# Optimization experiments

Measured on AMD Instinct MI355X. Metric: run time of the kernel, lower is better.

The kernel has to match this reference:

```python
import jax, jax.numpy as jnp
import numpy as np
from jax import lax

GAMMA = 1.0
INF = 1000000.0  # matches the TF code's pseudo-infinity


def _pairwise_sq_dists(a, b):
    # ||a_i - b_j||^2 = ||a||^2 + ||b||^2 - 2 a.b ; avoids the [B,N,M,d] diff tensor
    a2 = jnp.sum(a * a, axis=-1)                      # (B, N)
    b2 = jnp.sum(b * b, axis=-1)                      # (B, M)
    ab = jnp.einsum('bnd,bmd->bnm', a, b)             # (B, N, M)
    return a2[:, :, None] + b2[:, None, :] - 2.0 * ab


def _soft_dtw(seq_a, seq_b, gamma):
    D = _pairwise_sq_dists(seq_a, seq_b)              # (B, N, M)
    B, N, M = D.shape
    dtype = D.dtype
    # row 0 of the DP table: R[0,0]=0, R[0,j>0]=INF
    row0 = jnp.full((B, M + 1), INF, dtype=dtype).at[:, 0].set(0.0)

    def row_step(prev_row, d_i):
        # prev_row: (B, M+1) = R[i-1, :]; d_i: (B, M) = D[:, i-1, :]
        def col_step(left, inputs):
            diag, up, d = inputs                      # each (B,)
            r = jnp.stack([diag, up, left], axis=-1)  # (B, 3)
            softmin = -gamma * jax.nn.logsumexp(-r / gamma, axis=-1)
            val = d + softmin
            return val, val
        left0 = jnp.full((B,), INF, dtype=dtype)      # R[i, 0] = INF
        xs = (prev_row[:, :-1].T, prev_row[:, 1:].T, d_i.T)  # scan over M
        _, vals = lax.scan(col_step, left0, xs)       # (M, B)
        new_row = jnp.concatenate([jnp.full((B, 1), INF, dtype=dtype), vals.T], axis=1)
        return new_row, None

    final_row, _ = lax.scan(row_step, row0, jnp.moveaxis(D, 1, 0))
    return final_row[:, -1]                           # R[N, M]


def setup_inputs() -> dict:
    key = jax.random.key(0)
    k1, k2 = jax.random.split(key)
    B, N, M, d = 128, 384, 384, 128
    seq_a = jax.random.normal(k1, (B, N, d), dtype=jnp.float32)
    seq_b = jax.random.normal(k2, (B, M, d), dtype=jnp.float32)
    return {"seq_a": seq_a, "seq_b": seq_b}


def reference(seq_a, seq_b):
    dist = _soft_dtw(seq_a, seq_b, GAMMA)
    return dist[:, None]                              # (B, 1)
```

## Files before the change

kernel.cpp:

```cpp
#include <hip/hip_runtime.h>
#include <stdint.h>

#define BATCH 128
#define SEQN  384
#define SEQM  384
#define DIM   128
#define KINF   1000000.0f
#define LOG2E  1.4426950408889634f
#define LN2    0.6931471805599453f
#define KINF2  (KINF * LOG2E)
#define NCOLS  388

#define OFF1   162
#define SLACK  17
#define RBMASK 63

#define EXP2F(x) __builtin_amdgcn_exp2f(x)
#define LOG2F(x) __builtin_amdgcn_logf(x)

#define WG __HIP_MEMORY_SCOPE_WORKGROUP

typedef __attribute__((ext_vector_type(8))) short bf16x8;
typedef __attribute__((ext_vector_type(4))) float f32x4;

__device__ __forceinline__ unsigned short bf16_rne(float x) {
    uint32_t u = __float_as_uint(x);
    u += 0x7FFFu + ((u >> 16) & 1u);
    return (unsigned short)(u >> 16);
}
__device__ __forceinline__ uint32_t bf16_pair(float x, float y) {
    uint32_t ux = __float_as_uint(x); ux += 0x7FFFu + ((ux >> 16) & 1u);
    uint32_t uy = __float_as_uint(y); uy += 0x7FFFu + ((uy >> 16) & 1u);
    return (ux >> 16) | (uy & 0xFFFF0000u);
}

union frag_u { bf16x8 v; uint32_t u[4]; };
struct us3 { unsigned short u[3]; };

#define SPIN_NZ(addr)                                                        \
    { int g_ = 0;                                                            \
      while (__hip_atomic_load((addr), __ATOMIC_ACQUIRE, WG) == 0)           \
          if (++g_ > (1 << 20)) break; }
#define SPIN_GE(addr, val)                                                   \
    { int g_ = 0;                                                            \
      while (__hip_atomic_load((addr), __ATOMIC_ACQUIRE, WG) < (val))        \
          if (++g_ > (1 << 20)) break; }

__global__ __launch_bounds__(320) void fused_dtw(
        const float* __restrict__ A, const float* __restrict__ B,
        unsigned short* __restrict__ Dt, float* __restrict__ out) {
    __shared__ __align__(16) unsigned short ldsA[SEQN][DIM];
    __shared__ __align__(16) float normA[SEQN];
    __shared__ __align__(8)  float bring[128];
    __shared__ int prod_done[16];
    __shared__ int w0_prog, w1_prog, stage_cnt;

    const int bat  = blockIdx.x;
    const int tid  = threadIdx.x;
    const int wv   = tid >> 6;
    const int lane = tid & 63;

    if (tid < 16) prod_done[tid] = 0;
    if (tid == 16) w0_prog = -1;
    if (tid == 17) w1_prog = -1;
    if (tid == 18) stage_cnt = 0;
    __syncthreads();

    unsigned short* __restrict__ DtB = Dt + (long)bat * NCOLS * SEQN;

    if (wv >= 2) {
        const int pt = tid - 128;
        const float* __restrict__ Ab = A + (long)bat * SEQN * DIM;
        const float* __restrict__ Bb = B + (long)bat * SEQM * DIM;

        for (int sp = 0; sp < 8; sp++) {
            float4 v0[4], v1[4];
            #pragma unroll
            for (int j = 0; j < 4; j++) {
                int e = (sp * 4 + j) * 1536 + pt * 8;
                v0[j] = *(const float4*)(Ab + e);
                v1[j] = *(const float4*)(Ab + e + 4);
            }
            #pragma unroll
            for (int j = 0; j < 4; j++) {
                int e   = (sp * 4 + j) * 1536 + pt * 8;
                int row = e >> 7;
                int grp = (e >> 3) & 15;
                int sw  = (grp ^ (row & 15)) * 8;
                uint4 va;
                va.x = bf16_pair(v0[j].x, v0[j].y); va.y = bf16_pair(v0[j].z, v0[j].w);
                va.z = bf16_pair(v1[j].x, v1[j].y); va.w = bf16_pair(v1[j].z, v1[j].w);
                *(uint4*)&ldsA[row][sw] = va;
                float sa = v0[j].x*v0[j].x + v0[j].y*v0[j].y + v0[j].z*v0[j].z + v0[j].w*v0[j].w
                         + v1[j].x*v1[j].x + v1[j].y*v1[j].y + v1[j].z*v1[j].z + v1[j].w*v1[j].w;
                #pragma unroll
                for (int off = 8; off > 0; off >>= 1) sa += __shfl_down(sa, off, 16);
                if ((pt & 15) == 0) normA[row] = sa;
            }
        }
        if (lane == 0) __hip_atomic_fetch_add(&stage_cnt, 1, __ATOMIC_RELEASE, WG);
        SPIN_GE(&stage_cnt, 3);

        const int l16 = lane & 15, q = lane >> 4;
        for (int k = wv - 2; k < 13; k += 3) {
            if (k == 12) {
                uint32_t pv = bf16_pair(KINF2, KINF2);
                #pragma unroll
                for (int c = 0; c < 4; c++) {
                    uint32_t* p = (uint32_t*)(DtB + (long)(384 + c) * SEQN + 6 * lane);
                    p[0] = pv; p[1] = pv; p[2] = pv;
                }
            } else {
                frag_u bfrag[2][4];
                float bn[2];
                #pragma unroll
                for (int jg = 0; jg < 2; jg++) {
                    const float* bp = Bb + (long)(32 * k + jg * 16 + l16) * DIM + q * 8;
                    float s = 0.0f;
                    #pragma unroll
                    for (int kk = 0; kk < 4; kk++) {
                        float4 w0 = *(const float4*)(bp + kk * 32);
                        float4 w1 = *(const float4*)(bp + kk * 32 + 4);
                        bfrag[jg][kk].u[0] = bf16_pair(w0.x, w0.y);
                        bfrag[jg][kk].u[1] = bf16_pair(w0.z, w0.w);
                        bfrag[jg][kk].u[2] = bf16_pair(w1.x, w1.y);
                        bfrag[jg][kk].u[3] = bf16_pair(w1.z, w1.w);
                        s += w0.x*w0.x + w0.y*w0.y + w0.z*w0.z + w0.w*w0.w
                           + w1.x*w1.x + w1.y*w1.y + w1.z*w1.z + w1.w*w1.w;
                    }
                    s += __shfl_xor(s, 16, 64);
                    s += __shfl_xor(s, 32, 64);
                    bn[jg] = s;
                }
                for (int si = 0; si < 24; si++) {
                    const int arow = si * 16 + l16;
                    frag_u afr[4];
                    #pragma unroll
                    for (int kk = 0; kk < 4; kk++)
                        afr[kk].v = *(const bf16x8*)&ldsA[arow][((kk * 4 + q) ^ (arow & 15)) * 8];
                    f32x4 acc0 = {0.0f, 0.0f, 0.0f, 0.0f};
                    f32x4 acc1 = {0.0f, 0.0f, 0.0f, 0.0f};
                    #pragma unroll
                    for (int kk = 0; kk < 4; kk++) {
                        acc0 = __builtin_amdgcn_mfma_f32_16x16x32_bf16(
                                   afr[kk].v, bfrag[0][kk].v, acc0, 0, 0, 0);
                        acc1 = __builtin_amdgcn_mfma_f32_16x16x32_bf16(
                                   afr[kk].v, bfrag[1][kk].v, acc1, 0, 0, 0);
                    }
                    float4 an = *(const float4*)&normA[si * 16 + q * 4];
                    #pragma unroll
                    for (int jg = 0; jg < 2; jg++) {
                        int col = 32 * k + jg * 16 + l16;
                        f32x4 ac = jg ? acc1 : acc0;
                        ushort4 pk;
                        pk.x = bf16_rne((an.x + bn[jg] - 2.0f * ac[0]) * LOG2E);
                        pk.y = bf16_rne((an.y + bn[jg] - 2.0f * ac[1]) * LOG2E);
                        pk.z = bf16_rne((an.z + bn[jg] - 2.0f * ac[2]) * LOG2E);
                        pk.w = bf16_rne((an.w + bn[jg] - 2.0f * ac[3]) * LOG2E);
                        *(ushort4*)(DtB + (long)col * SEQN + si * 16 + q * 4) = pk;
                    }
                }
            }
            if (lane == 0)
                __hip_atomic_store(&prod_done[k], 1, __ATOMIC_RELEASE, WG);
        }
        return;
    }

    const int  cw    = wv;
    const int  t     = lane;
    const bool isl0  = (t == 0);
    const int  off   = cw ? OFF1 : 0;
    const int  npair = cw ? 168 : 160;
    const unsigned short* __restrict__ dtb = DtB + 192 * cw + 3 * t;

    SPIN_NZ(&prod_done[0]);

    float prev[3];
    #pragma unroll
    for (int r = 0; r < 3; r++) prev[r] = KINF2;

    us3 dslot[4];
    #pragma unroll
    for (int qq = 0; qq < 4; qq++) {
        int c = qq - 2 * t - off;
        int cc = c < 0 ? 0 : c;
        long base = (long)cc * SEQN;
        dslot[qq].u[0] = dtb[base];
        dslot[qq].u[1] = dtb[base + 1];
        dslot[qq].u[2] = dtb[base + 2];
    }

    float rcv0 = KINF2, rcv1 = KINF2, old_diag = KINF2;
    float lane0_diag = cw ? KINF2 : 0.0f;
    float b_rcv0 = KINF2, b_rcv1 = KINF2, b_old = KINF2;
    float botA = KINF2, botB = KINF2;
    int c0 = -2 * t - off;
    int kdone = 0;

#define UNPACK3(d, w)                                                       \
    d[0] = __uint_as_float(((uint32_t)w.u[0]) << 16);                       \
    d[1] = __uint_as_float(((uint32_t)w.u[1]) << 16);                       \
    d[2] = __uint_as_float(((uint32_t)w.u[2]) << 16);

#define COLPASS(dX, diag0, upseed, LEFTV, NEWV)                             \
    {                                                                       \
        float Bp = (upseed), Fp = 1.0f;                                     \
        float Bv[3], Fv[3];                                                 \
        _Pragma("unroll")                                                   \
        for (int r = 0; r < 3; r++) {                                       \
            float vd = (r == 0) ? (diag0) : LEFTV[r - 1];                   \
            float vl = LEFTV[r];                                            \
            float m3 = fminf(fminf(vd, vl), Bp);            \
            float al = EXP2F(m3 - Bp);                                      \
            float be = EXP2F(m3 - vd) + EXP2F(m3 - vl);                     \
            float Fr = __builtin_fmaf(al, Fp, be);                          \
            float Br = dX[r] + m3;                                          \
            Bv[r] = Br; Fv[r] = Fr;                                         \
            Bp = Br; Fp = Fr;                                               \
        }                                                                   \
        _Pragma("unroll")                                                   \
        for (int r = 0; r < 3; r++)                                         \
            NEWV[r] = Bv[r] - LOG2F(Fv[r]);                                 \
    }

#define PHASE2(Q)                                                           \
    {                                                                       \
        us3 wA = dslot[Q];                                                  \
        us3 wB = dslot[(Q) + 1];                                            \
        {                \
            int cnA = c0 + 4;                                               \
            int ccA = cnA < 0 ? 0 : (cnA > 387 ? 387 : cnA);                \
            int cnB = c0 + 5;                                               \
            int ccB = cnB < 0 ? 0 : (cnB > 387 ? 387 : cnB);                \
            long bA = (long)ccA * SEQN;                                     \
            long bB = (long)ccB * SEQN;                                     \
            dslot[Q].u[0]       = dtb[bA];                                  \
            dslot[Q].u[1]       = dtb[bA + 1];                              \
            dslot[Q].u[2]       = dtb[bA + 2];                              \
            dslot[(Q) + 1].u[0] = dtb[bB];                                  \
            dslot[(Q) + 1].u[1] = dtb[bB + 1];                              \
            dslot[(Q) + 1].u[2] = dtb[bB + 2];                              \
        }                                                                   \
        float dA[3], dB[3];                                                 \
        UNPACK3(dA, wA)                                                     \
        UNPACK3(dB, wB)                                                     \
        float dgA = isl0 ? (cw ? b_old  : lane0_diag) : old_diag;           \
        float upA = isl0 ? (cw ? b_rcv0 : KINF2)      : rcv0;               \
        float upB = isl0 ? (cw ? b_rcv1 : KINF2)      : rcv1;               \
        float newA[3];                                                      \
        COLPASS(dA, dgA, upA, prev, newA)                                   \
        COLPASS(dB, upA, upB, newA, prev)                                   \
        old_diag = rcv1;                                                    \
        rcv0 = __shfl_up(newA[2], 1, 64);                                   \
        rcv1 = __shfl_up(prev[2], 1, 64);                                   \
        botA = newA[2]; botB = prev[2];                                     \
        lane0_diag = KINF2;                                                 \
        c0 += 2;                                                            \
    }

#define TAIL0(m)                                                            \
    {                                                                       \
        if (t == 63) {                                                      \
            *(float2*)&bring[((m) & RBMASK) * 2] = make_float2(botA, botB); \
            if (((m) & 7) == 7)                                             \
                __hip_atomic_store(&w0_prog, (m), __ATOMIC_RELEASE, WG);    \
        }                                                                   \
    }
#define TAIL1(n)                                                            \
    {                                                                       \
        b_old = b_rcv1;                                                     \
        if ((n) >= SLACK) {                                                 \
            float2 bv = *(float2*)&bring[(((n) - SLACK) & RBMASK) * 2];     \
            b_rcv0 = bv.x; b_rcv1 = bv.y;                                   \
        } else { b_rcv0 = KINF2; b_rcv1 = KINF2; }                          \
        if (((n) & 7) == 7 && t == 63)                                      \
            __hip_atomic_store(&w1_prog, (n), __ATOMIC_RELEASE, WG);        \
    }

    for (int p = 0; p < npair; p++) {
        if ((p & 3) == 3) {
            int kr = (4 * p + 19 - off) >> 5;
            if (kr > 12) kr = 12;
            if (kr > kdone) { SPIN_NZ(&prod_done[kr]); kdone = kr; }
            if (cw) {
                int thr = 2 * p - 10;
                if (thr > 318) thr = 318;
                if (thr >= 0) SPIN_GE(&w0_prog, thr);
            } else {
                int thr = 2 * p - 40;
                if (thr >= 0) SPIN_GE(&w1_prog, thr);
            }
        }
        PHASE2(0)
        if (cw == 0) TAIL0(2 * p) else TAIL1(2 * p)
        PHASE2(2)
        if (cw == 0) TAIL0(2 * p + 1) else TAIL1(2 * p + 1)
    }
#undef PHASE2
#undef COLPASS
#undef UNPACK3
#undef TAIL0
#undef TAIL1

    if (cw == 1 && t == 63) out[bat] = prev[2] * LN2;
}

extern "C" void kernel_launch(void* const* d_in, const int* in_sizes, int n_in,
                              void* d_out, int out_size, void* d_ws, size_t ws_size,
                              hipStream_t stream) {
    (void)in_sizes; (void)n_in; (void)out_size; (void)ws_size;
    const float* a = (const float*)d_in[0];
    const float* b = (const float*)d_in[1];
    float* out = (float*)d_out;

    unsigned short* Dmat = (unsigned short*)d_ws;

    fused_dtw<<<dim3(BATCH), dim3(320), 0, stream>>>(a, b, Dmat, out);
}
```

Baseline: 218.9 us.

## Split each batch's DTW across two workgroups with global boundary exchange

```diff
diff --git a/kernel.cpp b/kernel.cpp
--- a/kernel.cpp
+++ b/kernel.cpp
@@ -9,16 +9,18 @@
 #define LOG2E  1.4426950408889634f
 #define LN2    0.6931471805599453f
 #define KINF2  (KINF * LOG2E)
-#define NCOLS  388
-
+
+#define HCOLS  388
+#define CSTR   200
 #define OFF1   162
 #define SLACK  17
-#define RBMASK 63
+#define BND_SLOTS 512
 
 #define EXP2F(x) __builtin_amdgcn_exp2f(x)
 #define LOG2F(x) __builtin_amdgcn_logf(x)
 
 #define WG __HIP_MEMORY_SCOPE_WORKGROUP
+#define AG __HIP_MEMORY_SCOPE_AGENT
 
 typedef __attribute__((ext_vector_type(8))) short bf16x8;
 typedef __attribute__((ext_vector_type(4))) float f32x4;
@@ -36,79 +38,43 @@
 
 union frag_u { bf16x8 v; uint32_t u[4]; };
 struct us3 { unsigned short u[3]; };
-
-#define SPIN_NZ(addr)                                                        \
-    { int g_ = 0;                                                            \
-      while (__hip_atomic_load((addr), __ATOMIC_ACQUIRE, WG) == 0)           \
-          if (++g_ > (1 << 20)) break; }
-#define SPIN_GE(addr, val)                                                   \
-    { int g_ = 0;                                                            \
-      while (__hip_atomic_load((addr), __ATOMIC_ACQUIRE, WG) < (val))        \
-          if (++g_ > (1 << 20)) break; }
-
-__global__ __launch_bounds__(320) void fused_dtw(
+union BU { float2 f; unsigned long long u; };
+
+__global__ __launch_bounds__(256) void fused_dtw(
         const float* __restrict__ A, const float* __restrict__ B,
-        unsigned short* __restrict__ Dt, float* __restrict__ out) {
-    __shared__ __align__(16) unsigned short ldsA[SEQN][DIM];
-    __shared__ __align__(16) float normA[SEQN];
-    __shared__ __align__(8)  float bring[128];
+        unsigned long long* __restrict__ bnd, int* __restrict__ w0prog,
+        float* __restrict__ out) {
+    __shared__ __align__(16) unsigned short ldsD[HCOLS * CSTR];
+    __shared__ __align__(16) float normA[192];
     __shared__ int prod_done[16];
-    __shared__ int w0_prog, w1_prog, stage_cnt;
-
-    const int bat  = blockIdx.x;
+
+    const int bx   = blockIdx.x;
+    const int bat  = bx >> 1;
+    const int h    = bx & 1;
     const int tid  = threadIdx.x;
     const int wv   = tid >> 6;
     const int lane = tid & 63;
 
     if (tid < 16) prod_done[tid] = 0;
-    if (tid == 16) w0_prog = -1;
-    if (tid == 17) w1_prog = -1;
-    if (tid == 18) stage_cnt = 0;
     __syncthreads();
 
-    unsigned short* __restrict__ DtB = Dt + (long)bat * NCOLS * SEQN;
-
-    if (wv >= 2) {
-        const int pt = tid - 128;
-        const float* __restrict__ Ab = A + (long)bat * SEQN * DIM;
+    unsigned long long* __restrict__ bndB = bnd + (long)bat * BND_SLOTS;
+    int* __restrict__ w0p = w0prog + bat;
+
+    if (wv != 0) {
+        const int l16 = lane & 15, q = lane >> 4;
+        const int sbase = (wv - 1) * 4;
+        const float* __restrict__ Ab = A + ((long)bat * SEQN + 192 * h) * DIM;
         const float* __restrict__ Bb = B + (long)bat * SEQM * DIM;
-
-        for (int sp = 0; sp < 8; sp++) {
-            float4 v0[4], v1[4];
-            #pragma unroll
-            for (int j = 0; j < 4; j++) {
-                int e = (sp * 4 + j) * 1536 + pt * 8;
-                v0[j] = *(const float4*)(Ab + e);
-                v1[j] = *(const float4*)(Ab + e + 4);
-            }
-            #pragma unroll
-            for (int j = 0; j < 4; j++) {
-                int e   = (sp * 4 + j) * 1536 + pt * 8;
-                int row = e >> 7;
-                int grp = (e >> 3) & 15;
-                int sw  = (grp ^ (row & 15)) * 8;
-                uint4 va;
-                va.x = bf16_pair(v0[j].x, v0[j].y); va.y = bf16_pair(v0[j].z, v0[j].w);
-                va.z = bf16_pair(v1[j].x, v1[j].y); va.w = bf16_pair(v1[j].z, v1[j].w);
-                *(uint4*)&ldsA[row][sw] = va;
-                float sa = v0[j].x*v0[j].x + v0[j].y*v0[j].y + v0[j].z*v0[j].z + v0[j].w*v0[j].w
-                         + v1[j].x*v1[j].x + v1[j].y*v1[j].y + v1[j].z*v1[j].z + v1[j].w*v1[j].w;
-                #pragma unroll
-                for (int off = 8; off > 0; off >>= 1) sa += __shfl_down(sa, off, 16);
-                if ((pt & 15) == 0) normA[row] = sa;
-            }
-        }
-        if (lane == 0) __hip_atomic_fetch_add(&stage_cnt, 1, __ATOMIC_RELEASE, WG);
-        SPIN_GE(&stage_cnt, 3);
-
-        const int l16 = lane & 15, q = lane >> 4;
-        for (int k = wv - 2; k < 13; k += 3) {
+        bool first = true;
+        for (int k = 0; k < 13; k++) {
             if (k == 12) {
-                uint32_t pv = bf16_pair(KINF2, KINF2);
-                #pragma unroll
-                for (int c = 0; c < 4; c++) {
-                    uint32_t* p = (uint32_t*)(DtB + (long)(384 + c) * SEQN + 6 * lane);
-                    p[0] = pv; p[1] = pv; p[2] = pv;
+                if (wv == 1) {
+                    uint32_t pv = bf16_pair(KINF2, KINF2);
+                    int c = lane >> 4, i16 = lane & 15;
+                    uint32_t* p = (uint32_t*)&ldsD[(384 + c) * CSTR] + i16 * 6;
+                    #pragma unroll
+                    for (int j = 0; j < 6; j++) p[j] = pv;
                 }
             } else {
                 frag_u bfrag[2][4];
@@ -132,12 +98,47 @@
                     s += __shfl_xor(s, 32, 64);
                     bn[jg] = s;
                 }
-                for (int si = 0; si < 24; si++) {
-                    const int arow = si * 16 + l16;
+                float4 c0v[4], c1v[4];
+                {
+                    const float* ap = Ab + (long)(sbase * 16 + l16) * DIM + q * 8;
+                    #pragma unroll
+                    for (int kk = 0; kk < 4; kk++) {
+                        c0v[kk] = *(const float4*)(ap + kk * 32);
+                        c1v[kk] = *(const float4*)(ap + kk * 32 + 4);
+                    }
+                }
+                #pragma unroll
+                for (int s4 = 0; s4 < 4; s4++) {
+                    const int si = sbase + s4;
+                    float4 n0[4], n1[4];
+                    if (s4 < 3) {
+                        const float* ap = Ab + (long)((si + 1) * 16 + l16) * DIM + q * 8;
+                        #pragma unroll
+                        for (int kk = 0; kk < 4; kk++) {
+                            n0[kk] = *(const float4*)(ap + kk * 32);
+                            n1[kk] = *(const float4*)(ap + kk * 32 + 4);
+                        }
+                    }
                     frag_u afr[4];
                     #pragma unroll
-                    for (int kk = 0; kk < 4; kk++)
-                        afr[kk].v = *(const bf16x8*)&ldsA[arow][((kk * 4 + q) ^ (arow & 15)) * 8];
+                    for (int kk = 0; kk < 4; kk++) {
+                        afr[kk].u[0] = bf16_pair(c0v[kk].x, c0v[kk].y);
+                        afr[kk].u[1] = bf16_pair(c0v[kk].z, c0v[kk].w);
+                        afr[kk].u[2] = bf16_pair(c1v[kk].x, c1v[kk].y);
+                        afr[kk].u[3] = bf16_pair(c1v[kk].z, c1v[kk].w);
+                    }
+                    if (first) {
+                        float sa = 0.0f;
+                        #pragma unroll
+                        for (int kk = 0; kk < 4; kk++)
+                            sa += c0v[kk].x*c0v[kk].x + c0v[kk].y*c0v[kk].y
+                                + c0v[kk].z*c0v[kk].z + c0v[kk].w*c0v[kk].w
+                                + c1v[kk].x*c1v[kk].x + c1v[kk].y*c1v[kk].y
+                                + c1v[kk].z*c1v[kk].z + c1v[kk].w*c1v[kk].w;
+                        sa += __shfl_xor(sa, 16, 64);
+                        sa += __shfl_xor(sa, 32, 64);
+                        if (q == 0) normA[si * 16 + l16] = sa;
+                    }
                     f32x4 acc0 = {0.0f, 0.0f, 0.0f, 0.0f};
                     f32x4 acc1 = {0.0f, 0.0f, 0.0f, 0.0f};
                     #pragma unroll
@@ -147,6 +148,7 @@
                         acc1 = __builtin_amdgcn_mfma_f32_16x16x32_bf16(
                                    afr[kk].v, bfrag[1][kk].v, acc1, 0, 0, 0);
                     }
+                    if (first) asm volatile("s_waitcnt lgkmcnt(0)" ::: "memory");
                     float4 an = *(const float4*)&normA[si * 16 + q * 4];
                     #pragma unroll
                     for (int jg = 0; jg < 2; jg++) {
@@ -157,24 +159,30 @@
                         pk.y = bf16_rne((an.y + bn[jg] - 2.0f * ac[1]) * LOG2E);
                         pk.z = bf16_rne((an.z + bn[jg] - 2.0f * ac[2]) * LOG2E);
                         pk.w = bf16_rne((an.w + bn[jg] - 2.0f * ac[3]) * LOG2E);
-                        *(ushort4*)(DtB + (long)col * SEQN + si * 16 + q * 4) = pk;
-                    }
-                }
+                        *(ushort4*)&ldsD[col * CSTR + si * 16 + q * 4] = pk;
+                    }
+                    if (s4 < 3) {
+                        #pragma unroll
+                        for (int kk = 0; kk < 4; kk++) { c0v[kk] = n0[kk]; c1v[kk] = n1[kk]; }
+                    }
+                }
+                first = false;
             }
             if (lane == 0)
-                __hip_atomic_store(&prod_done[k], 1, __ATOMIC_RELEASE, WG);
+                __hip_atomic_fetch_add(&prod_done[k], 1, __ATOMIC_RELEASE, WG);
         }
         return;
     }
 
-    const int  cw    = wv;
     const int  t     = lane;
     const bool isl0  = (t == 0);
-    const int  off   = cw ? OFF1 : 0;
-    const int  npair = cw ? 168 : 160;
-    const unsigned short* __restrict__ dtb = DtB + 192 * cw + 3 * t;
-
-    SPIN_NZ(&prod_done[0]);
+    const int  off   = h ? OFF1 : 0;
+    const int  npair = h ? 168 : 160;
+    const unsigned short* __restrict__ ldsT = ldsD + 3 * t;
+
+    {   int g = 0;
+        while (__hip_atomic_load(&prod_done[0], __ATOMIC_ACQUIRE, WG) < 3)
+            if (++g > (1 << 20)) break; }
 
     float prev[3];
     #pragma unroll
@@ -185,18 +193,18 @@
     for (int qq = 0; qq < 4; qq++) {
         int c = qq - 2 * t - off;
         int cc = c < 0 ? 0 : c;
-        long base = (long)cc * SEQN;
-        dslot[qq].u[0] = dtb[base];
-        dslot[qq].u[1] = dtb[base + 1];
-        dslot[qq].u[2] = dtb[base + 2];
+        const unsigned short* p = ldsT + cc * CSTR;
+        dslot[qq].u[0] = p[0]; dslot[qq].u[1] = p[1]; dslot[qq].u[2] = p[2];
     }
 
     float rcv0 = KINF2, rcv1 = KINF2, old_diag = KINF2;
-    float lane0_diag = cw ? KINF2 : 0.0f;
+    float lane0_diag = h ? KINF2 : 0.0f;
     float b_rcv0 = KINF2, b_rcv1 = KINF2, b_old = KINF2;
     float botA = KINF2, botB = KINF2;
+    float2 bq0, bq1, bq2, bq3;
+    bq0 = bq1 = bq2 = bq3 = make_float2(KINF2, KINF2);
     int c0 = -2 * t - off;
-    int kdone = 0;
+    int kdone = 0, w0seen = -1;
 
 #define UNPACK3(d, w)                                                       \
     d[0] = __uint_as_float(((uint32_t)w.u[0]) << 16);                       \
@@ -228,26 +236,26 @@
     {                                                                       \
         us3 wA = dslot[Q];                                                  \
         us3 wB = dslot[(Q) + 1];                                            \
-        {                \
+        {                     \
             int cnA = c0 + 4;                                               \
             int ccA = cnA < 0 ? 0 : (cnA > 387 ? 387 : cnA);                \
             int cnB = c0 + 5;                                               \
             int ccB = cnB < 0 ? 0 : (cnB > 387 ? 387 : cnB);                \
-            long bA = (long)ccA * SEQN;                                     \
-            long bB = (long)ccB * SEQN;                                     \
-            dslot[Q].u[0]       = dtb[bA];                                  \
-            dslot[Q].u[1]       = dtb[bA + 1];                              \
-            dslot[Q].u[2]       = dtb[bA + 2];                              \
-            dslot[(Q) + 1].u[0] = dtb[bB];                                  \
-            dslot[(Q) + 1].u[1] = dtb[bB + 1];                              \
-            dslot[(Q) + 1].u[2] = dtb[bB + 2];                              \
+            const unsigned short* pA = ldsT + ccA * CSTR;                   \
+            const unsigned short* pB = ldsT + ccB * CSTR;                   \
+            dslot[Q].u[0]       = pA[0];                                    \
+            dslot[Q].u[1]       = pA[1];                                    \
+            dslot[Q].u[2]       = pA[2];                                    \
+            dslot[(Q) + 1].u[0] = pB[0];                                    \
+            dslot[(Q) + 1].u[1] = pB[1];                                    \
+            dslot[(Q) + 1].u[2] = pB[2];                                    \
         }                                                                   \
         float dA[3], dB[3];                                                 \
         UNPACK3(dA, wA)                                                     \
         UNPACK3(dB, wB)                                                     \
-        float dgA = isl0 ? (cw ? b_old  : lane0_diag) : old_diag;           \
-        float upA = isl0 ? (cw ? b_rcv0 : KINF2)      : rcv0;               \
-        float upB = isl0 ? (cw ? b_rcv1 : KINF2)      : rcv1;               \
+        float dgA = isl0 ? (h ? b_old  : lane0_diag) : old_diag;            \
+        float upA = isl0 ? (h ? b_rcv0 : KINF2)      : rcv0;                \
+        float upB = isl0 ? (h ? b_rcv1 : KINF2)      : rcv1;                \
         float newA[3];                                                      \
         COLPASS(dA, dgA, upA, prev, newA)                                   \
         COLPASS(dB, upA, upB, newA, prev)                                   \
@@ -262,40 +270,52 @@
 #define TAIL0(m)                                                            \
     {                                                                       \
         if (t == 63) {                                                      \
-            *(float2*)&bring[((m) & RBMASK) * 2] = make_float2(botA, botB); \
+            BU bu; bu.f = make_float2(botA, botB);                          \
+            __hip_atomic_store(&bndB[m], bu.u, __ATOMIC_RELAXED, AG);       \
             if (((m) & 7) == 7)                                             \
-                __hip_atomic_store(&w0_prog, (m), __ATOMIC_RELEASE, WG);    \
+                __hip_atomic_store(w0p, (m), __ATOMIC_RELEASE, AG);         \
         }                                                                   \
     }
 #define TAIL1(n)                                                            \
     {                                                                       \
         b_old = b_rcv1;                                                     \
-        if ((n) >= SLACK) {                                                 \
-            float2 bv = *(float2*)&bring[(((n) - SLACK) & RBMASK) * 2];     \
-            b_rcv0 = bv.x; b_rcv1 = bv.y;                                   \
-        } else { b_rcv0 = KINF2; b_rcv1 = KINF2; }                          \
-        if (((n) & 7) == 7 && t == 63)                                      \
-            __hip_atomic_store(&w1_prog, (n), __ATOMIC_RELEASE, WG);        \
+        if ((n) >= SLACK) { b_rcv0 = bq0.x; b_rcv1 = bq0.y; }               \
+        else              { b_rcv0 = KINF2; b_rcv1 = KINF2; }               \
+        bq0 = bq1; bq1 = bq2; bq2 = bq3;                                    \
+        int sl = (n) + 4 - SLACK;                                           \
+        if (sl >= 0) {                                                      \
+            BU bu;                                                          \
+            bu.u = __hip_atomic_load(&bndB[sl], __ATOMIC_RELAXED, AG);      \
+            bq3 = bu.f;                                                     \
+        }                                                                   \
     }
 
     for (int p = 0; p < npair; p++) {
         if ((p & 3) == 3) {
             int kr = (4 * p + 19 - off) >> 5;
             if (kr > 12) kr = 12;
-            if (kr > kdone) { SPIN_NZ(&prod_done[kr]); kdone = kr; }
-            if (cw) {
-                int thr = 2 * p - 10;
-                if (thr > 318) thr = 318;
-                if (thr >= 0) SPIN_GE(&w0_prog, thr);
-            } else {
-                int thr = 2 * p - 40;
-                if (thr >= 0) SPIN_GE(&w1_prog, thr);
+            if (kr > kdone) {
+                int g = 0;
+                while (__hip_atomic_load(&prod_done[kr], __ATOMIC_ACQUIRE, WG) < 3)
+                    if (++g > (1 << 20)) break;
+                kdone = kr;
+            }
+            if (h) {
+                int thr = 2 * p - 6;
+                if (thr > 319) thr = 319;
+                if (thr >= 0 && w0seen < thr) {
+                    int g = 0, v = w0seen;
+                    do {
+                        v = __hip_atomic_load(w0p, __ATOMIC_ACQUIRE, AG);
+                    } while (v < thr && ++g < (1 << 20));
+                    w0seen = v;
+                }
             }
         }
         PHASE2(0)
-        if (cw == 0) TAIL0(2 * p) else TAIL1(2 * p)
+        if (h == 0) { TAIL0(2 * p) } else { TAIL1(2 * p) }
         PHASE2(2)
-        if (cw == 0) TAIL0(2 * p + 1) else TAIL1(2 * p + 1)
+        if (h == 0) { TAIL0(2 * p + 1) } else { TAIL1(2 * p + 1) }
     }
 #undef PHASE2
 #undef COLPASS
@@ -303,7 +323,7 @@
 #undef TAIL0
 #undef TAIL1
 
-    if (cw == 1 && t == 63) out[bat] = prev[2] * LN2;
+    if (h == 1 && t == 63) out[bat] = prev[2] * LN2;
 }
 
 extern "C" void kernel_launch(void* const* d_in, const int* in_sizes, int n_in,
@@ -314,7 +334,9 @@
     const float* b = (const float*)d_in[1];
     float* out = (float*)d_out;
 
-    unsigned short* Dmat = (unsigned short*)d_ws;
-
-    fused_dtw<<<dim3(BATCH), dim3(320), 0, stream>>>(a, b, Dmat, out);
+    unsigned long long* bnd = (unsigned long long*)d_ws;
+    int* w0prog = (int*)((char*)d_ws + (size_t)BATCH * BND_SLOTS * 8);
+
+    hipMemsetAsync(w0prog, 0xFF, BATCH * sizeof(int), stream);
+    fused_dtw<<<dim3(2 * BATCH), dim3(256), 0, stream>>>(a, b, bnd, w0prog, out);
 }
```

After: 337.1 us. 1.54x slower.
